# Kernel tuning notes

Measured on AMD Instinct MI355X. Metric: run time of the kernel, lower is better.

The kernel has to match this reference:

```python
import jax, jax.numpy as jnp
import numpy as np

EMBED_DIM = 512
N_HEADS = 8
HEAD_DIM = EMBED_DIM // N_HEADS
B, S = 4, 2048

def gelu(x):
    # torch F.gelu default = exact erf gelu
    return jax.nn.gelu(x, approximate=False)

def setup_inputs() -> dict:
    key = jax.random.key(0)
    ks = jax.random.split(key, 9)
    sc = 1.0 / np.sqrt(EMBED_DIM)
    inp = {
        'x':   jax.random.normal(ks[0], (B, S, EMBED_DIM), dtype=jnp.float32),
        'Wq':  jax.random.uniform(ks[1], (EMBED_DIM, EMBED_DIM), jnp.float32, -sc, sc),
        'bq':  jax.random.uniform(ks[2], (EMBED_DIM,), jnp.float32, -sc, sc),
        'Wk':  jax.random.uniform(ks[3], (EMBED_DIM, EMBED_DIM), jnp.float32, -sc, sc),
        'bk':  jax.random.uniform(ks[4], (EMBED_DIM,), jnp.float32, -sc, sc),
        'Wv':  jax.random.uniform(ks[5], (EMBED_DIM, EMBED_DIM), jnp.float32, -sc, sc),
        'bv':  jax.random.uniform(ks[6], (EMBED_DIM,), jnp.float32, -sc, sc),
        'Wo':  jax.random.uniform(ks[7], (EMBED_DIM, EMBED_DIM), jnp.float32, -sc, sc),
        'bo':  jax.random.uniform(ks[8], (EMBED_DIM,), jnp.float32, -sc, sc),
    }
    return inp

def reference(x, Wq, bq, Wk, bk, Wv, bv, Wo, bo):
    Bsz, Ssz, _ = x.shape
    def proj(W, b):
        # [B,S,E] -> [B,H,S,D], GELU applied before head split (same math either way)
        h = gelu(jnp.einsum('bse,ef->bsf', x, W.T) + b)
        return h.reshape(Bsz, Ssz, N_HEADS, HEAD_DIM).transpose(0, 2, 1, 3)
    q = proj(Wq, bq)
    k = proj(Wk, bk)
    v = proj(Wv, bv)
    attn = jnp.einsum('bhid,bhjd->bhij', q, k) / np.sqrt(HEAD_DIM).astype(np.float32)
    attn = jax.nn.softmax(attn, axis=-1)
    o = jnp.einsum('bhij,bhjd->bhid', attn, v)
    o = o.transpose(0, 2, 1, 3).reshape(Bsz, Ssz, EMBED_DIM)
    return gelu(jnp.einsum('bse,ef->bsf', o, Wo.T) + bo)
```

## Files before the change

kernel.cpp:

```cpp
#include <hip/hip_runtime.h>
#include <hip/hip_bf16.h>

typedef __bf16 bf16_t;
typedef __bf16 bf16x4 __attribute__((ext_vector_type(4)));
typedef __bf16 bf16x8 __attribute__((ext_vector_type(8)));
typedef float  f32x4  __attribute__((ext_vector_type(4)));
typedef float  f32x8  __attribute__((ext_vector_type(8)));

#define EMBED 512
#define NH    8
#define HD    64
#define SEQ   2048
#define MTOT  8192
#define SCQ   0.18033688011112042f

__device__ __forceinline__ float gelu_f(float x) {
    return 0.5f * x * (1.0f + erff(x * 0.7071067811865475f));
}

__device__ __forceinline__ f32x4 mfma16(bf16x8 a, bf16x8 b, f32x4 c) {
    return __builtin_amdgcn_mfma_f32_16x16x32_bf16(a, b, c, 0, 0, 0);
}

__global__ __launch_bounds__(256)
void convert_kernel(const float* __restrict__ x,  const float* __restrict__ Wq,
                    const float* __restrict__ Wk, const float* __restrict__ Wv,
                    bf16_t* __restrict__ xb, bf16_t* __restrict__ wb)
{
    const int y = blockIdx.y;
    const float* src; bf16_t* dst;
    if (y < 16)      { src = x + (size_t)y * 262144; dst = xb + (size_t)y * 262144; }
    else if (y == 16){ src = Wq; dst = wb; }
    else if (y == 17){ src = Wk; dst = wb + 262144; }
    else             { src = Wv; dst = wb + 524288; }
    const int base = (blockIdx.x * 256 + threadIdx.x) * 16;
    const f32x8 a = *(const f32x8*)(src + base);
    const f32x8 b = *(const f32x8*)(src + base + 8);
    *(bf16x8*)(dst + base)     = __builtin_convertvector(a, bf16x8);
    *(bf16x8*)(dst + base + 8) = __builtin_convertvector(b, bf16x8);
}

template<int MODE, int NTILE>
__global__ __launch_bounds__(256, 3)
void gemm_gelu_kernel(const bf16_t* __restrict__ Xb,
                      const bf16_t* __restrict__ Wb,
                      const float*  __restrict__ Wf,
                      const float*  __restrict__ Bq, const float* __restrict__ Bk,
                      const float*  __restrict__ Bv,
                      bf16_t* __restrict__ O0, bf16_t* __restrict__ O1,
                      bf16_t* __restrict__ O2, float* __restrict__ Of)
{
    constexpr int NTN = NTILE / 32;
    __shared__ __align__(16) bf16_t As[128 * 72];
    __shared__ __align__(16) bf16_t Bs[NTILE * 72];
    const int tid  = threadIdx.x;
    const int lane = tid & 63, w = tid >> 6, quad = lane >> 4, l15 = lane & 15;
    const int m0 = blockIdx.x * 128;
    int mat, n0;
    if (MODE == 0) { mat = blockIdx.y >> 2; n0 = (blockIdx.y & 3) * NTILE; }
    else           { mat = 0;               n0 = blockIdx.y * NTILE; }
    const bf16_t* W  = (MODE == 0) ? (Wb + (size_t)mat * 262144) : nullptr;
    const float*  Bi = (MODE == 1) ? Bq : (mat == 0 ? Bq : (mat == 1 ? Bk : Bv));

    const int wr = (w >> 1) * 64;
    const int wc = (w & 1) * (NTILE / 2);

    const int srow = tid >> 3, scol = (tid & 7) * 8;

    f32x4 acc[4][NTN];
#pragma unroll
    for (int a = 0; a < 4; ++a)
#pragma unroll
        for (int b = 0; b < NTN; ++b) acc[a][b] = f32x4{0.f, 0.f, 0.f, 0.f};

    bf16x8 xp[4];
    bf16x8 wpb[NTN];
    f32x8  wpf[NTN];

#pragma unroll
    for (int it = 0; it < 4; ++it)
        xp[it] = *(const bf16x8*)(Xb + (size_t)(m0 + it * 32 + srow) * EMBED + scol);
#pragma unroll
    for (int it = 0; it < NTN; ++it) {
        const int r = it * 32 + srow;
        if (MODE == 0) wpb[it] = *(const bf16x8*)(W + (size_t)(n0 + r) * EMBED + scol);
        else           wpf[it] = *(const f32x8*)(Wf + (size_t)(n0 + r) * EMBED + scol);
    }

#pragma unroll 1
    for (int kt = 0; kt < 8; ++kt) {
        __syncthreads();
#pragma unroll
        for (int it = 0; it < 4; ++it)
            *(bf16x8*)(As + (it * 32 + srow) * 72 + scol) = xp[it];
#pragma unroll
        for (int it = 0; it < NTN; ++it) {
            const int r = it * 32 + srow;
            if (MODE == 0) *(bf16x8*)(Bs + r * 72 + scol) = wpb[it];
            else *(bf16x8*)(Bs + r * 72 + scol) = __builtin_convertvector(wpf[it], bf16x8);
        }
        if (kt < 7) {
            const int k1 = (kt + 1) * 64;
#pragma unroll
            for (int it = 0; it < 4; ++it)
                xp[it] = *(const bf16x8*)(Xb + (size_t)(m0 + it * 32 + srow) * EMBED + k1 + scol);
#pragma unroll
            for (int it = 0; it < NTN; ++it) {
                const int r = it * 32 + srow;
                if (MODE == 0) wpb[it] = *(const bf16x8*)(W + (size_t)(n0 + r) * EMBED + k1 + scol);
                else           wpf[it] = *(const f32x8*)(Wf + (size_t)(n0 + r) * EMBED + k1 + scol);
            }
        }
        __syncthreads();
#pragma unroll
        for (int ks = 0; ks < 2; ++ks) {
            const int ko = (ks * 4 + quad) * 8;
            bf16x8 av[4], bv[NTN];
#pragma unroll
            for (int mt = 0; mt < 4; ++mt)
                av[mt] = *(const bf16x8*)(As + (wr + mt * 16 + l15) * 72 + ko);
#pragma unroll
            for (int nt = 0; nt < NTN; ++nt)
                bv[nt] = *(const bf16x8*)(Bs + (wc + nt * 16 + l15) * 72 + ko);
#pragma unroll
            for (int mt = 0; mt < 4; ++mt)
#pragma unroll
                for (int nt = 0; nt < NTN; ++nt)
                    acc[mt][nt] = mfma16(av[mt], bv[nt], acc[mt][nt]);
        }
    }

    float biasv[NTN];
#pragma unroll
    for (int nt = 0; nt < NTN; ++nt)
        biasv[nt] = Bi[n0 + wc + nt * 16 + l15];
#pragma unroll
    for (int mt = 0; mt < 4; ++mt) {
        const int mb = m0 + wr + mt * 16 + quad * 4;
        const int bb = mb >> 11, s0 = mb & (SEQ - 1);
#pragma unroll
        for (int nt = 0; nt < NTN; ++nt) {
            const int fc = n0 + wc + nt * 16 + l15;
            const int h = fc >> 6, d = fc & 63;
            float vv[4];
#pragma unroll
            for (int i = 0; i < 4; ++i) vv[i] = gelu_f(acc[mt][nt][i] + biasv[nt]);
            if (MODE == 1) {
#pragma unroll
                for (int i = 0; i < 4; ++i) Of[(size_t)(mb + i) * EMBED + fc] = vv[i];
            } else if (mat == 0) {
#pragma unroll
                for (int i = 0; i < 4; ++i)
                    O0[(((size_t)(bb * NH + h)) * SEQ + s0 + i) * HD + d] = (bf16_t)(vv[i] * SCQ);
            } else if (mat == 1) {
#pragma unroll
                for (int i = 0; i < 4; ++i)
                    O1[(((size_t)(bb * NH + h)) * SEQ + s0 + i) * HD + d] = (bf16_t)vv[i];
            } else {
                bf16x4 pk;
#pragma unroll
                for (int i = 0; i < 4; ++i) pk[i] = (bf16_t)vv[i];
                *(bf16x4*)(O2 + ((size_t)(bb * NH + h) * HD + d) * SEQ + s0) = pk;
            }
        }
    }
}

__global__ __launch_bounds__(256, 2)
void flash_attn_kernel(const bf16_t* __restrict__ Q,
                       const bf16_t* __restrict__ K,
                       const bf16_t* __restrict__ Vt,
                       bf16_t* __restrict__ Og)
{
    __shared__ __align__(16) bf16_t Ks[2][64 * 64];
    __shared__ __align__(16) bf16_t Vs[2][64 * 64];
    __shared__ __align__(16) bf16_t Ps[4][2][16 * 64];

    const int tid  = threadIdx.x;
    const int lane = tid & 63, w = tid >> 6, quad = lane >> 4, l15 = lane & 15;
    const int bh = blockIdx.y;
    const int q0 = blockIdx.x * 128;
    const size_t baseQK = (size_t)bh * SEQ * HD;
    const size_t baseV  = (size_t)bh * HD * SEQ;
    const int wm = w * 32;
    const int cx = (l15 & 7) << 3;

    bf16x8 qf0[2], qf1[2];
#pragma unroll
    for (int ks = 0; ks < 2; ++ks) {
        qf0[ks] = *(const bf16x8*)(Q + baseQK + (size_t)(q0 + wm + l15) * HD + ks * 32 + quad * 8);
        qf1[ks] = *(const bf16x8*)(Q + baseQK + (size_t)(q0 + wm + 16 + l15) * HD + ks * 32 + quad * 8);
    }

    f32x4 lacc0 = f32x4{0.f, 0.f, 0.f, 0.f};
    f32x4 lacc1 = f32x4{0.f, 0.f, 0.f, 0.f};
    f32x4 oacc0[4], oacc1[4];
#pragma unroll
    for (int nt = 0; nt < 4; ++nt) {
        oacc0[nt] = f32x4{0.f, 0.f, 0.f, 0.f};
        oacc1[nt] = f32x4{0.f, 0.f, 0.f, 0.f};
    }

    bf16_t* Pw0 = Ps[w][0];
    bf16_t* Pw1 = Ps[w][1];
    const int r0 = tid >> 3, c0 = (tid & 7) * 8;
    const int sA = (r0 << 6) + (c0 ^ ((r0 & 7) << 3));
    bf16x8 kr0, kr1, vr0, vr1;

    kr0 = *(const bf16x8*)(K + baseQK + (size_t)r0 * HD + c0);
    kr1 = *(const bf16x8*)(K + baseQK + (size_t)(r0 + 32) * HD + c0);
    vr0 = *(const bf16x8*)(Vt + baseV + (size_t)r0 * SEQ + c0);
    vr1 = *(const bf16x8*)(Vt + baseV + (size_t)(r0 + 32) * SEQ + c0);
    *(bf16x8*)(Ks[0] + sA)        = kr0;
    *(bf16x8*)(Ks[0] + sA + 2048) = kr1;
    *(bf16x8*)(Vs[0] + sA)        = vr0;
    *(bf16x8*)(Vs[0] + sA + 2048) = vr1;
    kr0 = *(const bf16x8*)(K + baseQK + (size_t)(64 + r0) * HD + c0);
    kr1 = *(const bf16x8*)(K + baseQK + (size_t)(64 + r0 + 32) * HD + c0);
    vr0 = *(const bf16x8*)(Vt + baseV + (size_t)r0 * SEQ + 64 + c0);
    vr1 = *(const bf16x8*)(Vt + baseV + (size_t)(r0 + 32) * SEQ + 64 + c0);

#pragma unroll 1
    for (int t = 0; t < 32; ++t) {
        __syncthreads();
        if (t + 1 < 32) {
            bf16_t* Kn = Ks[(t + 1) & 1];
            bf16_t* Vn = Vs[(t + 1) & 1];
            *(bf16x8*)(Kn + sA)        = kr0;
            *(bf16x8*)(Kn + sA + 2048) = kr1;
            *(bf16x8*)(Vn + sA)        = vr0;
            *(bf16x8*)(Vn + sA + 2048) = vr1;
        }
        if (t + 2 < 32) {
            const int kv = (t + 2) * 64;
            kr0 = *(const bf16x8*)(K + baseQK + (size_t)(kv + r0) * HD + c0);
            kr1 = *(const bf16x8*)(K + baseQK + (size_t)(kv + r0 + 32) * HD + c0);
            vr0 = *(const bf16x8*)(Vt + baseV + (size_t)r0 * SEQ + kv + c0);
            vr1 = *(const bf16x8*)(Vt + baseV + (size_t)(r0 + 32) * SEQ + kv + c0);
        }

        const bf16_t* Kb = Ks[t & 1];
        const bf16_t* Vb = Vs[t & 1];

        f32x4 sf0[4], sf1[4];
#pragma unroll
        for (int jt = 0; jt < 4; ++jt) {
            sf0[jt] = f32x4{0.f, 0.f, 0.f, 0.f};
            sf1[jt] = f32x4{0.f, 0.f, 0.f, 0.f};
        }
        __builtin_amdgcn_s_setprio(1);
#pragma unroll
        for (int ks = 0; ks < 2; ++ks) {
            const int ko = (ks * 32 + quad * 8) ^ cx;
#pragma unroll
            for (int jt = 0; jt < 4; ++jt) {
                const bf16x8 a = *(const bf16x8*)(Kb + ((jt * 16 + l15) << 6) + ko);
                sf0[jt] = mfma16(a, qf0[ks], sf0[jt]);
                sf1[jt] = mfma16(a, qf1[ks], sf1[jt]);
            }
        }
        __builtin_amdgcn_s_setprio(0);

#pragma unroll
        for (int jt = 0; jt < 4; ++jt) {
#pragma unroll
            for (int i = 0; i < 4; ++i) sf0[jt][i] = exp2f(sf0[jt][i] - 8.f);
            lacc0 += sf0[jt];
            const bf16x4 pk = __builtin_convertvector(sf0[jt], bf16x4);
            *(bf16x4*)(Pw0 + (l15 << 6) + ((jt * 16 + quad * 4) ^ cx)) = pk;
        }
#pragma unroll
        for (int jt = 0; jt < 4; ++jt) {
#pragma unroll
            for (int i = 0; i < 4; ++i) sf1[jt][i] = exp2f(sf1[jt][i] - 8.f);
            lacc1 += sf1[jt];
            const bf16x4 pk = __builtin_convertvector(sf1[jt], bf16x4);
            *(bf16x4*)(Pw1 + (l15 << 6) + ((jt * 16 + quad * 4) ^ cx)) = pk;
        }

        __builtin_amdgcn_s_setprio(1);
#pragma unroll
        for (int c = 0; c < 2; ++c) {
            const int ko = (c * 32 + quad * 8) ^ cx;
            const bf16x8 pa0 = *(const bf16x8*)(Pw0 + (l15 << 6) + ko);
            const bf16x8 pa1 = *(const bf16x8*)(Pw1 + (l15 << 6) + ko);
#pragma unroll
            for (int nt = 0; nt < 4; ++nt) {
                const bf16x8 b = *(const bf16x8*)(Vb + ((nt * 16 + l15) << 6) + ko);
                oacc0[nt] = mfma16(pa0, b, oacc0[nt]);
                oacc1[nt] = mfma16(pa1, b, oacc1[nt]);
            }
        }
        __builtin_amdgcn_s_setprio(0);
    }

    const int bidx = bh >> 3, h = bh & 7;
#pragma unroll
    for (int g = 0; g < 2; ++g) {
        const f32x4 la = g ? lacc1 : lacc0;
        const f32x4* oa = g ? oacc1 : oacc0;
        float rs = (la[0] + la[1]) + (la[2] + la[3]);
        rs += __shfl_xor(rs, 16);
        rs += __shfl_xor(rs, 32);
        float lf[4];
#pragma unroll
        for (int i = 0; i < 4; ++i)
            lf[i] = __shfl(rs, (lane & 48) | (quad * 4 + i));
#pragma unroll
        for (int nt = 0; nt < 4; ++nt)
#pragma unroll
            for (int i = 0; i < 4; ++i) {
                const int s = q0 + wm + g * 16 + quad * 4 + i;
                const int d = nt * 16 + l15;
                Og[((size_t)(bidx * SEQ + s)) * EMBED + h * HD + d] =
                    (bf16_t)(oa[nt][i] / lf[i]);
            }
    }
}

extern "C" void kernel_launch(void* const* d_in, const int* in_sizes, int n_in,
                              void* d_out, int out_size, void* d_ws, size_t ws_size,
                              hipStream_t stream)
{
    const float* x  = (const float*)d_in[0];
    const float* Wq = (const float*)d_in[1];
    const float* bq = (const float*)d_in[2];
    const float* Wk = (const float*)d_in[3];
    const float* bk = (const float*)d_in[4];
    const float* Wv = (const float*)d_in[5];
    const float* bv = (const float*)d_in[6];
    const float* Wo = (const float*)d_in[7];
    const float* bo = (const float*)d_in[8];
    float* out = (float*)d_out;

    const size_t NE = (size_t)MTOT * EMBED;
    bf16_t* xb  = (bf16_t*)d_out;
    bf16_t* Qw  = (bf16_t*)d_out + NE;
    bf16_t* Kw  = (bf16_t*)d_ws;
    bf16_t* Vtw = Kw + NE;
    bf16_t* Ow  = Vtw + NE;
    bf16_t* Wb  = Ow;

    convert_kernel<<<dim3(64, 19), 256, 0, stream>>>(x, Wq, Wk, Wv, xb, Wb);
    gemm_gelu_kernel<0, 128><<<dim3(64, 12), 256, 0, stream>>>(
        xb, Wb, nullptr, bq, bk, bv, Qw, Kw, Vtw, nullptr);
    flash_attn_kernel<<<dim3(16, 32), 256, 0, stream>>>(Qw, Kw, Vtw, Ow);
    gemm_gelu_kernel<1, 64><<<dim3(64, 8), 256, 0, stream>>>(
        Ow, nullptr, Wo, bo, nullptr, nullptr, nullptr, nullptr, nullptr, out);
}
```

Measured before the change: 185.3 us.

## Deepen attention K/V prefetch to distance three and use non-draining barriers

Adds a barrier that waits only on LDS counters, not outstanding global loads, and uses it in the projection GEMM and the attention loop. This lets global prefetches stay in flight across barriers. The attention loop is unrolled by two with alternating register sets, so K/V tiles are fetched three iterations ahead instead of two. The cost is more VGPRs for the extra prefetch registers, which may pressure occupancy under launch_bounds(256,2), plus correctness now depends on the compiler inserting vmcnt waits before the register data is used.

Result: no change. 183.3 us (-1.0%).

```diff
diff --git a/kernel.cpp b/kernel.cpp
--- a/kernel.cpp
+++ b/kernel.cpp
@@ -20,6 +20,12 @@
 
 __device__ __forceinline__ f32x4 mfma16(bf16x8 a, bf16x8 b, f32x4 c) {
     return __builtin_amdgcn_mfma_f32_16x16x32_bf16(a, b, c, 0, 0, 0);
+}
+
+__device__ __forceinline__ void barrier_nodrain() {
+    asm volatile("s_waitcnt lgkmcnt(0)" ::: "memory");
+    __builtin_amdgcn_s_barrier();
+    asm volatile("" ::: "memory");
 }
 
 __global__ __launch_bounds__(256)
@@ -89,7 +95,7 @@
 
 #pragma unroll 1
     for (int kt = 0; kt < 8; ++kt) {
-        __syncthreads();
+        barrier_nodrain();
 #pragma unroll
         for (int it = 0; it < 4; ++it)
             *(bf16x8*)(As + (it * 32 + srow) * 72 + scol) = xp[it];
@@ -111,7 +117,7 @@
                 else           wpf[it] = *(const f32x8*)(Wf + (size_t)(n0 + r) * EMBED + k1 + scol);
             }
         }
-        __syncthreads();
+        barrier_nodrain();
 #pragma unroll
         for (int ks = 0; ks < 2; ++ks) {
             const int ko = (ks * 4 + quad) * 8;
@@ -165,6 +171,76 @@
         }
     }
 }
+
+#define FA_ITER(T, BUF, KR0, KR1, VR0, VR1)                                   \
+    do {                                                                      \
+        if ((T) + 1 < 32) {                                                   \
+            bf16_t* Kn = Ks[(BUF) ^ 1];                                       \
+            bf16_t* Vn = Vs[(BUF) ^ 1];                                       \
+            *(bf16x8*)(Kn + sA)        = KR0;                                 \
+            *(bf16x8*)(Kn + sA + 2048) = KR1;                                 \
+            *(bf16x8*)(Vn + sA)        = VR0;                                 \
+            *(bf16x8*)(Vn + sA + 2048) = VR1;                                 \
+        }                                                                     \
+        if ((T) + 3 < 32) {                                                   \
+            const int kv = ((T) + 3) * 64;                                    \
+            KR0 = *(const bf16x8*)(K + baseQK + (size_t)(kv + r0) * HD + c0); \
+            KR1 = *(const bf16x8*)(K + baseQK + (size_t)(kv + r0 + 32) * HD + c0); \
+            VR0 = *(const bf16x8*)(Vt + baseV + (size_t)r0 * SEQ + kv + c0);  \
+            VR1 = *(const bf16x8*)(Vt + baseV + (size_t)(r0 + 32) * SEQ + kv + c0); \
+        }                                                                     \
+        const bf16_t* Kb = Ks[(BUF)];                                         \
+        const bf16_t* Vb = Vs[(BUF)];                                         \
+        f32x4 sf0[4], sf1[4];                                                 \
+        _Pragma("unroll")                                                     \
+        for (int jt = 0; jt < 4; ++jt) {                                      \
+            sf0[jt] = f32x4{0.f, 0.f, 0.f, 0.f};                              \
+            sf1[jt] = f32x4{0.f, 0.f, 0.f, 0.f};                              \
+        }                                                                     \
+        __builtin_amdgcn_s_setprio(1);                                        \
+        _Pragma("unroll")                                                     \
+        for (int ks = 0; ks < 2; ++ks) {                                      \
+            const int ko = (ks * 32 + quad * 8) ^ cx;                         \
+            _Pragma("unroll")                                                 \
+            for (int jt = 0; jt < 4; ++jt) {                                  \
+                const bf16x8 a = *(const bf16x8*)(Kb + ((jt * 16 + l15) << 6) + ko); \
+                sf0[jt] = mfma16(a, qf0[ks], sf0[jt]);                        \
+                sf1[jt] = mfma16(a, qf1[ks], sf1[jt]);                        \
+            }                                                                 \
+        }                                                                     \
+        __builtin_amdgcn_s_setprio(0);                                        \
+        _Pragma("unroll")                                                     \
+        for (int jt = 0; jt < 4; ++jt) {                                      \
+            _Pragma("unroll")                                                 \
+            for (int i = 0; i < 4; ++i) sf0[jt][i] = exp2f(sf0[jt][i] - 8.f); \
+            lacc0 += sf0[jt];                                                 \
+            const bf16x4 pk = __builtin_convertvector(sf0[jt], bf16x4);       \
+            *(bf16x4*)(Pw0 + (l15 << 6) + ((jt * 16 + quad * 4) ^ cx)) = pk;  \
+        }                                                                     \
+        _Pragma("unroll")                                                     \
+        for (int jt = 0; jt < 4; ++jt) {                                      \
+            _Pragma("unroll")                                                 \
+            for (int i = 0; i < 4; ++i) sf1[jt][i] = exp2f(sf1[jt][i] - 8.f); \
+            lacc1 += sf1[jt];                                                 \
+            const bf16x4 pk = __builtin_convertvector(sf1[jt], bf16x4);       \
+            *(bf16x4*)(Pw1 + (l15 << 6) + ((jt * 16 + quad * 4) ^ cx)) = pk;  \
+        }                                                                     \
+        __builtin_amdgcn_s_setprio(1);                                        \
+        _Pragma("unroll")                                                     \
+        for (int c = 0; c < 2; ++c) {                                         \
+            const int ko = (c * 32 + quad * 8) ^ cx;                          \
+            const bf16x8 pa0 = *(const bf16x8*)(Pw0 + (l15 << 6) + ko);       \
+            const bf16x8 pa1 = *(const bf16x8*)(Pw1 + (l15 << 6) + ko);       \
+            _Pragma("unroll")                                                 \
+            for (int nt = 0; nt < 4; ++nt) {                                  \
+                const bf16x8 b = *(const bf16x8*)(Vb + ((nt * 16 + l15) << 6) + ko); \
+                oacc0[nt] = mfma16(pa0, b, oacc0[nt]);                        \
+                oacc1[nt] = mfma16(pa1, b, oacc1[nt]);                        \
+            }                                                                 \
+        }                                                                     \
+        __builtin_amdgcn_s_setprio(0);                                        \
+        if ((T) < 31) barrier_nodrain();                                      \
+    } while (0)
 
 __global__ __launch_bounds__(256, 2)
 void flash_attn_kernel(const bf16_t* __restrict__ Q,
@@ -205,93 +281,32 @@
     bf16_t* Pw1 = Ps[w][1];
     const int r0 = tid >> 3, c0 = (tid & 7) * 8;
     const int sA = (r0 << 6) + (c0 ^ ((r0 & 7) << 3));
-    bf16x8 kr0, kr1, vr0, vr1;
-
-    kr0 = *(const bf16x8*)(K + baseQK + (size_t)r0 * HD + c0);
-    kr1 = *(const bf16x8*)(K + baseQK + (size_t)(r0 + 32) * HD + c0);
-    vr0 = *(const bf16x8*)(Vt + baseV + (size_t)r0 * SEQ + c0);
-    vr1 = *(const bf16x8*)(Vt + baseV + (size_t)(r0 + 32) * SEQ + c0);
-    *(bf16x8*)(Ks[0] + sA)        = kr0;
-    *(bf16x8*)(Ks[0] + sA + 2048) = kr1;
-    *(bf16x8*)(Vs[0] + sA)        = vr0;
-    *(bf16x8*)(Vs[0] + sA + 2048) = vr1;
-    kr0 = *(const bf16x8*)(K + baseQK + (size_t)(64 + r0) * HD + c0);
-    kr1 = *(const bf16x8*)(K + baseQK + (size_t)(64 + r0 + 32) * HD + c0);
-    vr0 = *(const bf16x8*)(Vt + baseV + (size_t)r0 * SEQ + 64 + c0);
-    vr1 = *(const bf16x8*)(Vt + baseV + (size_t)(r0 + 32) * SEQ + 64 + c0);
+
+    bf16x8 kA0, kA1, vA0, vA1;
+    bf16x8 kB0, kB1, vB0, vB1;
+
+    kA0 = *(const bf16x8*)(K + baseQK + (size_t)r0 * HD + c0);
+    kA1 = *(const bf16x8*)(K + baseQK + (size_t)(r0 + 32) * HD + c0);
+    vA0 = *(const bf16x8*)(Vt + baseV + (size_t)r0 * SEQ + c0);
+    vA1 = *(const bf16x8*)(Vt + baseV + (size_t)(r0 + 32) * SEQ + c0);
+    *(bf16x8*)(Ks[0] + sA)        = kA0;
+    *(bf16x8*)(Ks[0] + sA + 2048) = kA1;
+    *(bf16x8*)(Vs[0] + sA)        = vA0;
+    *(bf16x8*)(Vs[0] + sA + 2048) = vA1;
+    kB0 = *(const bf16x8*)(K + baseQK + (size_t)(64 + r0) * HD + c0);
+    kB1 = *(const bf16x8*)(K + baseQK + (size_t)(64 + r0 + 32) * HD + c0);
+    vB0 = *(const bf16x8*)(Vt + baseV + (size_t)r0 * SEQ + 64 + c0);
+    vB1 = *(const bf16x8*)(Vt + baseV + (size_t)(r0 + 32) * SEQ + 64 + c0);
+    kA0 = *(const bf16x8*)(K + baseQK + (size_t)(128 + r0) * HD + c0);
+    kA1 = *(const bf16x8*)(K + baseQK + (size_t)(128 + r0 + 32) * HD + c0);
+    vA0 = *(const bf16x8*)(Vt + baseV + (size_t)r0 * SEQ + 128 + c0);
+    vA1 = *(const bf16x8*)(Vt + baseV + (size_t)(r0 + 32) * SEQ + 128 + c0);
+    barrier_nodrain();
 
 #pragma unroll 1
-    for (int t = 0; t < 32; ++t) {
-        __syncthreads();
-        if (t + 1 < 32) {
-            bf16_t* Kn = Ks[(t + 1) & 1];
-            bf16_t* Vn = Vs[(t + 1) & 1];
-            *(bf16x8*)(Kn + sA)        = kr0;
-            *(bf16x8*)(Kn + sA + 2048) = kr1;
-            *(bf16x8*)(Vn + sA)        = vr0;
-            *(bf16x8*)(Vn + sA + 2048) = vr1;
-        }
-        if (t + 2 < 32) {
-            const int kv = (t + 2) * 64;
-            kr0 = *(const bf16x8*)(K + baseQK + (size_t)(kv + r0) * HD + c0);
-            kr1 = *(const bf16x8*)(K + baseQK + (size_t)(kv + r0 + 32) * HD + c0);
-            vr0 = *(const bf16x8*)(Vt + baseV + (size_t)r0 * SEQ + kv + c0);
-            vr1 = *(const bf16x8*)(Vt + baseV + (size_t)(r0 + 32) * SEQ + kv + c0);
-        }
-
-        const bf16_t* Kb = Ks[t & 1];
-        const bf16_t* Vb = Vs[t & 1];
-
-        f32x4 sf0[4], sf1[4];
-#pragma unroll
-        for (int jt = 0; jt < 4; ++jt) {
-            sf0[jt] = f32x4{0.f, 0.f, 0.f, 0.f};
-            sf1[jt] = f32x4{0.f, 0.f, 0.f, 0.f};
-        }
-        __builtin_amdgcn_s_setprio(1);
-#pragma unroll
-        for (int ks = 0; ks < 2; ++ks) {
-            const int ko = (ks * 32 + quad * 8) ^ cx;
-#pragma unroll
-            for (int jt = 0; jt < 4; ++jt) {
-                const bf16x8 a = *(const bf16x8*)(Kb + ((jt * 16 + l15) << 6) + ko);
-                sf0[jt] = mfma16(a, qf0[ks], sf0[jt]);
-                sf1[jt] = mfma16(a, qf1[ks], sf1[jt]);
-            }
-        }
-        __builtin_amdgcn_s_setprio(0);
-
-#pragma unroll
-        for (int jt = 0; jt < 4; ++jt) {
-#pragma unroll
-            for (int i = 0; i < 4; ++i) sf0[jt][i] = exp2f(sf0[jt][i] - 8.f);
-            lacc0 += sf0[jt];
-            const bf16x4 pk = __builtin_convertvector(sf0[jt], bf16x4);
-            *(bf16x4*)(Pw0 + (l15 << 6) + ((jt * 16 + quad * 4) ^ cx)) = pk;
-        }
-#pragma unroll
-        for (int jt = 0; jt < 4; ++jt) {
-#pragma unroll
-            for (int i = 0; i < 4; ++i) sf1[jt][i] = exp2f(sf1[jt][i] - 8.f);
-            lacc1 += sf1[jt];
-            const bf16x4 pk = __builtin_convertvector(sf1[jt], bf16x4);
-            *(bf16x4*)(Pw1 + (l15 << 6) + ((jt * 16 + quad * 4) ^ cx)) = pk;
-        }
-
-        __builtin_amdgcn_s_setprio(1);
-#pragma unroll
-        for (int c = 0; c < 2; ++c) {
-            const int ko = (c * 32 + quad * 8) ^ cx;
-            const bf16x8 pa0 = *(const bf16x8*)(Pw0 + (l15 << 6) + ko);
-            const bf16x8 pa1 = *(const bf16x8*)(Pw1 + (l15 << 6) + ko);
-#pragma unroll
-            for (int nt = 0; nt < 4; ++nt) {
-                const bf16x8 b = *(const bf16x8*)(Vb + ((nt * 16 + l15) << 6) + ko);
-                oacc0[nt] = mfma16(pa0, b, oacc0[nt]);
-                oacc1[nt] = mfma16(pa1, b, oacc1[nt]);
-            }
-        }
-        __builtin_amdgcn_s_setprio(0);
+    for (int tt = 0; tt < 32; tt += 2) {
+        FA_ITER(tt,     0, kB0, kB1, vB0, vB1);
+        FA_ITER(tt + 1, 1, kA0, kA1, vA0, vA1);
     }
 
     const int bidx = bh >> 3, h = bh & 7;
```
